# Kernel optimization log

Hardware: AMD Instinct MI355X
Metric: run time of the kernel (lower is better)

Reference implementation:

```python
import jax, jax.numpy as jnp
import numpy as np

B = 65536
L = 128          # latent_dim
H = 20           # hidden_size of first LSTMCell
H2 = 2           # hidden_size of projection LSTMCell
NEG_SLOPE = 0.01 # F.leaky_relu default


def _uniform(k, shape, bound):
    return jax.random.uniform(k, shape, jnp.float32, -bound, bound)


def setup_inputs() -> dict:
    key = jax.random.key(0)
    ks = jax.random.split(key, 12)
    b1 = 1.0 / np.sqrt(H)
    b2 = 1.0 / np.sqrt(H2)
    return {
        "mu": jax.random.normal(ks[0], (B, L), jnp.float32),
        "log_var": jax.random.normal(ks[1], (B, L), jnp.float32),
        "eps0": jax.random.normal(ks[2], (B,), jnp.float32),
        "eps": jax.random.normal(ks[3], (L, B), jnp.float32),
        # lstm_unit: input_size=2, hidden=20 -> gates 4H
        "Wih1": _uniform(ks[4], (4 * H, 2), b1),
        "Whh1": _uniform(ks[5], (4 * H, H), b1),
        "bih1": _uniform(ks[6], (4 * H,), b1),
        "bhh1": _uniform(ks[7], (4 * H,), b1),
        # lstm_projection: input_size=2H, hidden=2 -> gates 4*2
        "Wih2": _uniform(ks[8], (4 * H2, 2 * H), b2),
        "Whh2": _uniform(ks[9], (4 * H2, H2), b2),
        "bih2": _uniform(ks[10], (4 * H2,), b2),
        "bhh2": _uniform(ks[11], (4 * H2,), b2),
    }


def _lstm_cell(x, h, c, Wih, Whh, bih, bhh):
    # torch.nn.LSTMCell: gates ordered i, f, g, o
    g = x @ Wih.T + h @ Whh.T + (bih + bhh)
    i, f, gg, o = jnp.split(g, 4, axis=1)
    c_new = jax.nn.sigmoid(f) * c + jax.nn.sigmoid(i) * jnp.tanh(gg)
    h_new = jax.nn.sigmoid(o) * jnp.tanh(c_new)
    return h_new, c_new


def reference(mu, log_var, eps0, eps,
              Wih1, Whh1, bih1, bhh1,
              Wih2, Whh2, bih2, bhh2):
    b = mu.shape[0]
    latent_dim = mu.shape[1]

    # initial reparameterized input from dim 0
    x0 = eps0 * jnp.exp(0.5 * log_var[:, 0]) + mu[:, 0]
    inp0 = jnp.stack([x0, jnp.zeros_like(x0)], axis=1)  # [B, 2]

    carry0 = (
        jnp.zeros((b, H), mu.dtype),   # hidden_state
        jnp.zeros((b, H), mu.dtype),   # cell_state
        jnp.zeros((b, H2), mu.dtype),  # hidden_state_second
        jnp.zeros((b, H2), mu.dtype),  # cell_state_second
        inp0,                          # current input [B, 2]
    )
    xs = (eps, mu.T, jnp.arange(latent_dim, dtype=mu.dtype))  # per-step [B], [B], []

    def step(carry, xs_t):
        h1, c1, h2, c2, x = carry
        eps_t, mu_t, idx = xs_t
        h1, c1 = _lstm_cell(x, h1, c1, Wih1, Whh1, bih1, bhh1)
        out1 = jax.nn.leaky_relu(jnp.concatenate([h1, c1], axis=1), NEG_SLOPE)
        h2, c2 = _lstm_cell(out1, h2, c2, Wih2, Whh2, bih2, bhh2)
        mu_r = h2[:, 0]
        lv_r = h2[:, 1]
        samp = eps_t * jnp.exp(0.5 * lv_r) + mu_r
        # sample=False: teacher-force next input from mu[:, idx]
        nxt = jnp.stack([mu_t, jnp.full_like(mu_t, 0.0) + idx], axis=1)
        return (h1, c1, h2, c2, nxt), (mu_r, lv_r, samp)

    _, (mus_r, lvs_r, samples) = jax.lax.scan(step, carry0, xs)
    # [L, B] -> [B, L]
    return mus_r.T, lvs_r.T, samples.T
```

## Files before the change

kernel.cpp:

```cpp
#include <hip/hip_runtime.h>

#define BB 65536
#define LL 128
#define HH 20
#define LOG2E 1.4426950408889634f

typedef __attribute__((ext_vector_type(8))) short  bf16x8;
typedef __attribute__((ext_vector_type(4))) float  f32x4;
typedef __attribute__((ext_vector_type(2))) float  f32x2;
typedef __attribute__((ext_vector_type(4))) int    i32x4;

__device__ __forceinline__ float frcp(float x)  { return __builtin_amdgcn_rcpf(x); }
__device__ __forceinline__ float ex2(float x)   { return __builtin_amdgcn_exp2f(x); }
__device__ __forceinline__ float lrelu(float x) { return fmaxf(x, 0.01f * x); }
__device__ __forceinline__ float csign(float mag, float sgn) {
    int m = __builtin_bit_cast(int, mag), s = __builtin_bit_cast(int, sgn);
    return __builtin_bit_cast(float, (m & 0x7fffffff) | (s & 0x80000000));
}
__device__ __forceinline__ unsigned cvt_pk(float lo, float hi) {
    unsigned r;
    asm("v_cvt_pk_bf16_f32 %0, %1, %2" : "=v"(r) : "v"(lo), "v"(hi));
    return r;
}
__device__ __forceinline__ bf16x8 pack8v(f32x4 a, f32x4 b) {
    i32x4 t = { (int)cvt_pk(a[0], a[1]), (int)cvt_pk(a[2], a[3]),
                (int)cvt_pk(b[0], b[1]), (int)cvt_pk(b[2], b[3]) };
    return __builtin_bit_cast(bf16x8, t);
}

__device__ __forceinline__ void lstm_unit(f32x4 a, float& c, float& h) {
    float ei  = ex2(-a[0]);
    float ef  = ex2(-a[1]);
    float eo  = ex2(-a[3]);
    float egm = ex2(-fabsf(a[2] + a[2]));
    float numg = 1.f - egm, deng = 1.f + egm;
    float A = 1.f + ef, B = 1.f + ei;
    float P = B * deng;
    float D = P * A;
    float n2 = csign(numg * A, a[2]);
    float cn = fmaf(c, P, n2) * frcp(D);
    c = cn;
    float ecm = ex2(-fabsf(cn * (2.f * LOG2E)));
    float numc = 1.f - ecm;
    float Do = (1.f + eo) * (1.f + ecm);
    h = csign(numc, cn) * frcp(Do);
}

__device__ __forceinline__ void lstm_unit2(f32x4 a0, f32x4 a1, f32x2& c, f32x2& h) {
    f32x2 gg = {a0[2], a1[2]};
    f32x2 ei  = {ex2(-a0[0]), ex2(-a1[0])};
    f32x2 ef  = {ex2(-a0[1]), ex2(-a1[1])};
    f32x2 eo  = {ex2(-a0[3]), ex2(-a1[3])};
    f32x2 tg  = gg + gg;
    f32x2 egm = {ex2(-fabsf(tg[0])), ex2(-fabsf(tg[1]))};
    f32x2 numg = 1.f - egm;
    f32x2 deng = 1.f + egm;
    f32x2 A = 1.f + ef, B = 1.f + ei;
    f32x2 P = B * deng;
    f32x2 D = P * A;
    f32x2 nA = numg * A;
    f32x2 n2 = {csign(nA[0], gg[0]), csign(nA[1], gg[1])};
    f32x2 rD = {frcp(D[0]), frcp(D[1])};
    f32x2 cn = (c * P + n2) * rD;
    c = cn;
    f32x2 tc = cn * (2.f * LOG2E);
    f32x2 ecm = {ex2(-fabsf(tc[0])), ex2(-fabsf(tc[1]))};
    f32x2 numc = 1.f - ecm;
    f32x2 Do = (1.f + eo) * (1.f + ecm);
    f32x2 rDo = {frcp(Do[0]), frcp(Do[1])};
    f32x2 sc = {csign(numc[0], cn[0]), csign(numc[1], cn[1])};
    h = sc * rDo;
}

__global__ __launch_bounds__(256) void sampler_lstm(
    const float* __restrict__ mu, const float* __restrict__ log_var,
    const float* __restrict__ eps0, const float* __restrict__ eps,
    const float* __restrict__ Wih1, const float* __restrict__ Whh1,
    const float* __restrict__ bih1, const float* __restrict__ bhh1,
    const float* __restrict__ Wih2, const float* __restrict__ Whh2,
    const float* __restrict__ bih2, const float* __restrict__ bhh2,
    float* __restrict__ out)
{
    __shared__ __align__(16) float st[4][16][52];
    __shared__ __align__(16) float ob[4][3][16][20];

    const int tid  = threadIdx.x;
    const int wave = tid >> 6;
    const int lane = tid & 63;
    const int b16  = lane & 15;
    const int q    = lane >> 4;
    const int gb0  = (blockIdx.x * 4 + wave) * 16;
    const int gb   = gb0 + b16;

    float (*stw)[52]     = st[wave];
    float (*obw)[16][20] = ob[wave];

    bf16x8 a1[5];
    #pragma unroll
    for (int T = 0; T < 5; ++T) {
        int G = 16 * T + b16;
        int j = G >> 2, g = G & 3;
        int row = g * HH + j;
        float v[8];
        #pragma unroll
        for (int e = 0; e < 8; ++e) {
            int k = 4 * q + (e & 3) + 16 * (e >> 2);
            float val;
            if (k < 20)       val = Whh1[row * HH + k];
            else if (k == 20) val = Wih1[row * 2 + 0];
            else if (k == 21) val = Wih1[row * 2 + 1];
            else if (k == 22) val = bih1[row] + bhh1[row];
            else              val = 0.f;
            v[e] = val * LOG2E;
        }
        f32x4 lo = {v[0], v[1], v[2], v[3]}, hi4 = {v[4], v[5], v[6], v[7]};
        a1[T] = pack8v(lo, hi4);
    }
    bf16x8 a2f[2];
    #pragma unroll
    for (int f = 0; f < 2; ++f) {
        float v[8];
        #pragma unroll
        for (int e = 0; e < 8; ++e) {
            int k = 32 * f + 4 * q + (e & 3) + 16 * (e >> 2);
            float val = 0.f;
            if (b16 < 8) {
                int u = b16 >> 2, p = b16 & 3;
                int ro = 2 * p + u;
                if (k < 20)       val = Wih2[ro * 40 + k];
                else if (k < 24)  val = 0.f;
                else if (k < 44)  val = Wih2[ro * 40 + 20 + (k - 24)];
                else if (k == 44) val = Whh2[ro * 2 + 0];
                else if (k == 45) val = Whh2[ro * 2 + 1];
                else if (k == 46) val = bih2[ro] + bhh2[ro];
            }
            v[e] = val * LOG2E;
        }
        f32x4 lo = {v[0], v[1], v[2], v[3]}, hi4 = {v[4], v[5], v[6], v[7]};
        a2f[f] = pack8v(lo, hi4);
    }

    const float* murow = mu + (size_t)gb * LL;
    float samp0 = eps0[gb] * ex2(0.5f * LOG2E * log_var[(size_t)gb * LL]) + murow[0];
    #pragma unroll
    for (int d = 0; d < 13; ++d) {
        int col = 13 * q + d;
        stw[b16][col] = (col == 20) ? samp0 : (col == 22 || col == 46) ? 1.f : 0.f;
    }

    const f32x4 kz = {0.f, 0.f, 0.f, 0.f};
    f32x2 c01 = {0.f, 0.f}, c23 = {0.f, 0.f};
    float c4 = 0.f, c2 = 0.f;

    bf16x8 b1;
    {
        f32x4 v0 = *reinterpret_cast<const f32x4*>(&stw[b16][4 * q]);
        f32x4 v1 = *reinterpret_cast<const f32x4*>(&stw[b16][16 + 4 * q]);
        b1 = pack8v(v0, v1);
    }

    #pragma unroll 1
    for (int tb = 0; tb < 8; ++tb) {
        #pragma unroll 2
        for (int ti = 0; ti < 16; ++ti) {
            const int t = tb * 16 + ti;
            const float mu_t  = murow[t];
            const float eps_t = eps[(size_t)t * BB + gb];

            f32x4 acc[5];
            #pragma unroll
            for (int T = 0; T < 5; ++T)
                acc[T] = __builtin_amdgcn_mfma_f32_16x16x32_bf16(a1[T], b1, kz, 0, 0, 0);

            f32x2 h01, h23;
            float h4;
            lstm_unit2(acc[0], acc[1], c01, h01);
            lstm_unit2(acc[2], acc[3], c23, h23);
            lstm_unit(acc[4], c4, h4);

            stw[b16][q]      = h01[0];
            stw[b16][4 + q]  = h01[1];
            stw[b16][8 + q]  = h23[0];
            stw[b16][12 + q] = h23[1];
            stw[b16][16 + q] = h4;
            stw[b16][24 + q] = c01[0];
            stw[b16][28 + q] = c01[1];
            stw[b16][32 + q] = c23[0];
            stw[b16][36 + q] = c23[1];
            stw[b16][40 + q] = c4;
            if (q == 1) { stw[b16][20] = mu_t; stw[b16][21] = (float)t; }

            f32x4 u0 = *reinterpret_cast<const f32x4*>(&stw[b16][4 * q]);
            f32x4 u1 = *reinterpret_cast<const f32x4*>(&stw[b16][16 + 4 * q]);
            f32x4 u2 = *reinterpret_cast<const f32x4*>(&stw[b16][32 + 4 * q]);
            b1 = pack8v(u0, u1);

            f32x4 l0, l1, l2;
            #pragma unroll
            for (int i = 0; i < 4; ++i) {
                l0[i] = lrelu(u0[i]);
                l1[i] = lrelu(u1[i]);
                l2[i] = (q < 3) ? lrelu(u2[i]) : u2[i];
            }
            bf16x8 b2a = pack8v(l0, l1);
            unsigned p0 = cvt_pk(l2[0], l2[1]), p1 = cvt_pk(l2[2], l2[3]);
            i32x4 tdup = {(int)p0, (int)p1, (int)p0, (int)p1};
            bf16x8 b2b = __builtin_bit_cast(bf16x8, tdup);

            f32x4 g2 = __builtin_amdgcn_mfma_f32_16x16x32_bf16(a2f[0], b2a, kz, 0, 0, 0);
            g2 = __builtin_amdgcn_mfma_f32_16x16x32_bf16(a2f[1], b2b, g2, 0, 0, 0);

            float h2;
            lstm_unit(g2, c2, h2);
            if (q < 2) stw[b16][44 + q] = h2;
            float h2o = __shfl_xor(h2, 16);

            if (q == 0) {
                obw[0][b16][ti] = h2;
                obw[1][b16][ti] = h2o;
                obw[2][b16][ti] = fmaf(eps_t, ex2(0.5f * LOG2E * h2o), h2);
            }
        }

        {
            int bq = lane >> 2, ch = lane & 3;
            #pragma unroll
            for (int o = 0; o < 3; ++o) {
                f32x4 v = *reinterpret_cast<const f32x4*>(&obw[o][bq][ch * 4]);
                float* dst = out + (size_t)o * BB * LL + (size_t)(gb0 + bq) * LL
                           + tb * 16 + ch * 4;
                *(float4*)dst = make_float4(v[0], v[1], v[2], v[3]);
            }
        }
    }
}

extern "C" void kernel_launch(void* const* d_in, const int* in_sizes, int n_in,
                              void* d_out, int out_size, void* d_ws, size_t ws_size,
                              hipStream_t stream) {
    sampler_lstm<<<dim3(BB / 64), dim3(256), 0, stream>>>(
        (const float*)d_in[0],  (const float*)d_in[1],  (const float*)d_in[2],
        (const float*)d_in[3],  (const float*)d_in[4],  (const float*)d_in[5],
        (const float*)d_in[6],  (const float*)d_in[7],  (const float*)d_in[8],
        (const float*)d_in[9],  (const float*)d_in[10], (const float*)d_in[11],
        (float*)d_out);
}
```

Measured before the change: 263.1 us.

## Re-layout LDS state rows for vectorized stores and split mu/eps loads by lane group

```diff
diff --git a/kernel.cpp b/kernel.cpp
--- a/kernel.cpp
+++ b/kernel.cpp
@@ -81,7 +81,7 @@
     const float* __restrict__ bih2, const float* __restrict__ bhh2,
     float* __restrict__ out)
 {
-    __shared__ __align__(16) float st[4][16][52];
+    __shared__ __align__(16) float st[4][16][68];
     __shared__ __align__(16) float ob[4][3][16][20];
 
     const int tid  = threadIdx.x;
@@ -92,7 +92,7 @@
     const int gb0  = (blockIdx.x * 4 + wave) * 16;
     const int gb   = gb0 + b16;
 
-    float (*stw)[52]     = st[wave];
+    float (*stw)[68]     = st[wave];
     float (*obw)[16][20] = ob[wave];
 
     bf16x8 a1[5];
@@ -104,13 +104,14 @@
         float v[8];
         #pragma unroll
         for (int e = 0; e < 8; ++e) {
-            int k = 4 * q + (e & 3) + 16 * (e >> 2);
-            float val;
-            if (k < 20)       val = Whh1[row * HH + k];
-            else if (k == 20) val = Wih1[row * 2 + 0];
-            else if (k == 21) val = Wih1[row * 2 + 1];
-            else if (k == 22) val = bih1[row] + bhh1[row];
-            else              val = 0.f;
+            float val = 0.f;
+            if (e < 4)        val = Whh1[row * HH + 4 * e + q];
+            else if (e == 4)  val = Whh1[row * HH + 16 + q];
+            else if (q == 0) {
+                if (e == 5)      val = Wih1[row * 2 + 0];
+                else if (e == 6) val = Wih1[row * 2 + 1];
+                else             val = bih1[row] + bhh1[row];
+            }
             v[e] = val * LOG2E;
         }
         f32x4 lo = {v[0], v[1], v[2], v[3]}, hi4 = {v[4], v[5], v[6], v[7]};
@@ -122,17 +123,22 @@
         float v[8];
         #pragma unroll
         for (int e = 0; e < 8; ++e) {
-            int k = 32 * f + 4 * q + (e & 3) + 16 * (e >> 2);
             float val = 0.f;
             if (b16 < 8) {
                 int u = b16 >> 2, p = b16 & 3;
                 int ro = 2 * p + u;
-                if (k < 20)       val = Wih2[ro * 40 + k];
-                else if (k < 24)  val = 0.f;
-                else if (k < 44)  val = Wih2[ro * 40 + 20 + (k - 24)];
-                else if (k == 44) val = Whh2[ro * 2 + 0];
-                else if (k == 45) val = Whh2[ro * 2 + 1];
-                else if (k == 46) val = bih2[ro] + bhh2[ro];
+                if (f == 0) {
+                    if (e < 4)       val = Wih2[ro * 40 + 4 * e + q];
+                    else if (e == 4) val = Wih2[ro * 40 + 16 + q];
+                } else {
+                    if (e < 4)       val = Wih2[ro * 40 + 20 + 4 * e + q];
+                    else if (e == 4) val = Wih2[ro * 40 + 36 + q];
+                    else if (q == 0) {
+                        if (e == 5)      val = Whh2[ro * 2 + 0];
+                        else if (e == 6) val = Whh2[ro * 2 + 1];
+                        else             val = bih2[ro] + bhh2[ro];
+                    }
+                }
             }
             v[e] = val * LOG2E;
         }
@@ -143,10 +149,11 @@
     const float* murow = mu + (size_t)gb * LL;
     float samp0 = eps0[gb] * ex2(0.5f * LOG2E * log_var[(size_t)gb * LL]) + murow[0];
     #pragma unroll
-    for (int d = 0; d < 13; ++d) {
-        int col = 13 * q + d;
-        stw[b16][col] = (col == 20) ? samp0 : (col == 22 || col == 46) ? 1.f : 0.f;
-    }
+    for (int d = 0; d < 17; ++d) stw[b16][17 * q + d] = 0.f;
+    if (q == 0) { stw[b16][5] = samp0; stw[b16][7] = 1.f; stw[b16][39] = 1.f; }
+
+    const float* rp = (q == 1) ? murow : (eps + gb);
+    const size_t rstride = (q == 1) ? 1 : (size_t)BB;
 
     const f32x4 kz = {0.f, 0.f, 0.f, 0.f};
     f32x2 c01 = {0.f, 0.f}, c23 = {0.f, 0.f};
@@ -154,8 +161,8 @@
 
     bf16x8 b1;
     {
-        f32x4 v0 = *reinterpret_cast<const f32x4*>(&stw[b16][4 * q]);
-        f32x4 v1 = *reinterpret_cast<const f32x4*>(&stw[b16][16 + 4 * q]);
+        f32x4 v0 = *reinterpret_cast<const f32x4*>(&stw[b16][8 * q]);
+        f32x4 v1 = *reinterpret_cast<const f32x4*>(&stw[b16][8 * q + 4]);
         b1 = pack8v(v0, v1);
     }
 
@@ -164,8 +171,8 @@
         #pragma unroll 2
         for (int ti = 0; ti < 16; ++ti) {
             const int t = tb * 16 + ti;
-            const float mu_t  = murow[t];
-            const float eps_t = eps[(size_t)t * BB + gb];
+            const float ldv = *rp;
+            rp += rstride;
 
             f32x4 acc[5];
             #pragma unroll
@@ -178,47 +185,45 @@
             lstm_unit2(acc[2], acc[3], c23, h23);
             lstm_unit(acc[4], c4, h4);
 
-            stw[b16][q]      = h01[0];
-            stw[b16][4 + q]  = h01[1];
-            stw[b16][8 + q]  = h23[0];
-            stw[b16][12 + q] = h23[1];
-            stw[b16][16 + q] = h4;
-            stw[b16][24 + q] = c01[0];
-            stw[b16][28 + q] = c01[1];
-            stw[b16][32 + q] = c23[0];
-            stw[b16][36 + q] = c23[1];
-            stw[b16][40 + q] = c4;
-            if (q == 1) { stw[b16][20] = mu_t; stw[b16][21] = (float)t; }
-
-            f32x4 u0 = *reinterpret_cast<const f32x4*>(&stw[b16][4 * q]);
-            f32x4 u1 = *reinterpret_cast<const f32x4*>(&stw[b16][16 + 4 * q]);
-            f32x4 u2 = *reinterpret_cast<const f32x4*>(&stw[b16][32 + 4 * q]);
+            f32x4 hv = {h01[0], h01[1], h23[0], h23[1]};
+            f32x4 cv = {c01[0], c01[1], c23[0], c23[1]};
+            *reinterpret_cast<f32x4*>(&stw[b16][8 * q]) = hv;
+            stw[b16][8 * q + 4] = h4;
+            *reinterpret_cast<f32x4*>(&stw[b16][32 + 8 * q]) = cv;
+            stw[b16][32 + 8 * q + 4] = c4;
+            if (q == 1) { stw[b16][5] = ldv; stw[b16][6] = (float)t; }
+
+            f32x4 u0 = *reinterpret_cast<const f32x4*>(&stw[b16][8 * q]);
+            f32x4 u1 = *reinterpret_cast<const f32x4*>(&stw[b16][8 * q + 4]);
+            f32x4 u2 = *reinterpret_cast<const f32x4*>(&stw[b16][32 + 8 * q]);
+            f32x4 u3 = *reinterpret_cast<const f32x4*>(&stw[b16][32 + 8 * q + 4]);
             b1 = pack8v(u0, u1);
 
-            f32x4 l0, l1, l2;
+            f32x4 l0, l1, l2, l3;
             #pragma unroll
             for (int i = 0; i < 4; ++i) {
                 l0[i] = lrelu(u0[i]);
                 l1[i] = lrelu(u1[i]);
-                l2[i] = (q < 3) ? lrelu(u2[i]) : u2[i];
-            }
+                l2[i] = lrelu(u2[i]);
+            }
+            l3[0] = lrelu(u3[0]);
+            l3[1] = u3[1]; l3[2] = u3[2]; l3[3] = u3[3];
+
             bf16x8 b2a = pack8v(l0, l1);
-            unsigned p0 = cvt_pk(l2[0], l2[1]), p1 = cvt_pk(l2[2], l2[3]);
-            i32x4 tdup = {(int)p0, (int)p1, (int)p0, (int)p1};
-            bf16x8 b2b = __builtin_bit_cast(bf16x8, tdup);
+            bf16x8 b2b = pack8v(l2, l3);
 
             f32x4 g2 = __builtin_amdgcn_mfma_f32_16x16x32_bf16(a2f[0], b2a, kz, 0, 0, 0);
             g2 = __builtin_amdgcn_mfma_f32_16x16x32_bf16(a2f[1], b2b, g2, 0, 0, 0);
 
             float h2;
             lstm_unit(g2, c2, h2);
-            if (q < 2) stw[b16][44 + q] = h2;
+            if (q < 2) stw[b16][37 + q] = h2;
             float h2o = __shfl_xor(h2, 16);
 
             if (q == 0) {
                 obw[0][b16][ti] = h2;
                 obw[1][b16][ti] = h2o;
-                obw[2][b16][ti] = fmaf(eps_t, ex2(0.5f * LOG2E * h2o), h2);
+                obw[2][b16][ti] = fmaf(ldv, ex2(0.5f * LOG2E * h2o), h2);
             }
         }
 
```

Result: faster. 257.2 us (-2.2%).
